# Kernel tuning notes

Hardware: AMD Instinct MI355X
Metric: run time of the kernel (lower is better)

## Reference

```python
import jax, jax.numpy as jnp
import numpy as np

VOCAB, HID, ADIM, B = 20, 128, 3, 32
NP, EP, NM, EM = 50000, 800000, 50000, 800000
IN_DIM = VOCAB + 3  # one-hot residues + 3D pos


def _gcn_conv(x, edge_index, W, b, n):
    # PyG GCNConv: h = XW; add self-loops; sym-normalized scatter-add; + bias
    h = x @ W
    loop = jnp.arange(n, dtype=edge_index.dtype)
    src = jnp.concatenate([edge_index[0], loop])
    dst = jnp.concatenate([edge_index[1], loop])
    deg = jax.ops.segment_sum(jnp.ones_like(dst, dtype=h.dtype), dst, num_segments=n)
    dinv = jnp.where(deg > 0, jax.lax.rsqrt(deg), 0.0)
    norm = dinv[src] * dinv[dst]  # [E+N]
    msg = h[src] * norm[:, None]  # [E+N, HID] dominant memory traffic
    return jax.ops.segment_sum(msg, dst, num_segments=n) + b


def _mean_pool(x, batch, nb):
    s = jax.ops.segment_sum(x, batch, num_segments=nb)
    c = jax.ops.segment_sum(jnp.ones((x.shape[0],), x.dtype), batch, num_segments=nb)
    return s / jnp.maximum(c, 1.0)[:, None]


def setup_inputs() -> dict:
    key = jax.random.key(0)
    ks = jax.random.split(key, 32)
    p = lambda k, shp: jax.random.normal(k, shp, dtype=jnp.float32) * 0.02
    inp = {
        "protein_residue": jax.random.randint(ks[0], (NP,), 0, VOCAB, dtype=jnp.int32),
        "protein_pos": jax.random.normal(ks[1], (NP, 3), dtype=jnp.float32),
        "protein_edge_index": jax.random.randint(ks[2], (2, EP), 0, NP, dtype=jnp.int32),
        "protein_batch": jnp.sort(jax.random.randint(ks[3], (NP,), 0, B, dtype=jnp.int32)),
        "molecule_residue": jax.random.randint(ks[4], (NM,), 0, VOCAB, dtype=jnp.int32),
        "molecule_pos": jax.random.normal(ks[5], (NM, 3), dtype=jnp.float32),
        "molecule_edge_index": jax.random.randint(ks[6], (2, EM), 0, NM, dtype=jnp.int32),
        "molecule_batch": jnp.sort(jax.random.randint(ks[7], (NM,), 0, B, dtype=jnp.int32)),
        "t": jax.random.randint(ks[8], (B,), 0, 1000, dtype=jnp.int32),
        "noisy_action": jax.random.normal(ks[9], (NM, ADIM), dtype=jnp.float32),
        # GCN params
        "Wp1": p(ks[10], (IN_DIM, HID)), "bp1": jnp.zeros((HID,), jnp.float32),
        "Wp2": p(ks[11], (HID, HID)),   "bp2": jnp.zeros((HID,), jnp.float32),
        "Wm1": p(ks[12], (IN_DIM, HID)), "bm1": jnp.zeros((HID,), jnp.float32),
        "Wm2": p(ks[13], (HID, HID)),   "bm2": jnp.zeros((HID,), jnp.float32),
        # timestep MLP
        "Wt1": p(ks[14], (1, HID)),   "bt1": jnp.zeros((HID,), jnp.float32),
        "Wt2": p(ks[15], (HID, HID)), "bt2": jnp.zeros((HID,), jnp.float32),
        # noise predictor: in = 2*HID + ADIM + HID = 387
        "Wn1": p(ks[16], (2 * HID + ADIM + HID, HID)), "bn1": jnp.zeros((HID,), jnp.float32),
        "Wn2": p(ks[17], (HID, ADIM)), "bn2": jnp.zeros((ADIM,), jnp.float32),
    }
    return inp


def reference(protein_residue, protein_pos, protein_edge_index, protein_batch,
              molecule_residue, molecule_pos, molecule_edge_index, molecule_batch,
              t, noisy_action,
              Wp1, bp1, Wp2, bp2, Wm1, bm1, Wm2, bm2,
              Wt1, bt1, Wt2, bt2, Wn1, bn1, Wn2, bn2):
    # protein branch
    x_p = jnp.concatenate([jax.nn.one_hot(protein_residue, VOCAB, dtype=jnp.float32), protein_pos], axis=1)
    x_p = jax.nn.relu(_gcn_conv(x_p, protein_edge_index, Wp1, bp1, NP))
    x_p = jax.nn.relu(_gcn_conv(x_p, protein_edge_index, Wp2, bp2, NP))
    protein_emb = _mean_pool(x_p, protein_batch, B)  # [B, HID]
    # molecule branch
    x_m = jnp.concatenate([jax.nn.one_hot(molecule_residue, VOCAB, dtype=jnp.float32), molecule_pos], axis=1)
    x_m = jax.nn.relu(_gcn_conv(x_m, molecule_edge_index, Wm1, bm1, NM))
    x_m = jax.nn.relu(_gcn_conv(x_m, molecule_edge_index, Wm2, bm2, NM))
    # timestep embedding
    t_emb = jax.nn.relu(t[:, None].astype(jnp.float32) @ Wt1 + bt1) @ Wt2 + bt2  # [B, HID]
    # gather pooled embeddings per molecule node, concat, MLP
    feat = jnp.concatenate([x_m, protein_emb[molecule_batch], t_emb[molecule_batch], noisy_action], axis=1)
    return jax.nn.relu(feat @ Wn1 + bn1) @ Wn2 + bn2  # [NM, ADIM]
```

## Files before the change

### kernel.cpp

```cpp
#include <hip/hip_runtime.h>
#include <hip/hip_bf16.h>

#define HID 128
#define BSH 7
#define CSRCAP 4096
#define PCHUNK 4096
#define HCHUNK 16384

typedef __attribute__((ext_vector_type(8))) short short8v;
typedef __attribute__((ext_vector_type(4))) float f32x4;
typedef __attribute__((ext_vector_type(2))) float f32x2;

#if defined(__has_builtin)
#if __has_builtin(__builtin_amdgcn_cvt_f32_fp8) && __has_builtin(__builtin_amdgcn_cvt_pk_fp8_f32)
#define HAVE_HW_FP8 1
#endif
#if __has_builtin(__builtin_amdgcn_cvt_pk_f32_fp8)
#define HAVE_HW_FP8_PK 1
#endif
#endif

__device__ __forceinline__ float4 f4fma(float a, float4 x, float4 y) {
    y.x += a * x.x; y.y += a * x.y; y.z += a * x.z; y.w += a * x.w; return y;
}
__device__ __forceinline__ unsigned f2bf2(float lo, float hi) {
    unsigned ul = __float_as_uint(lo), uh = __float_as_uint(hi);
    ul = (ul + 0x7FFF + ((ul >> 16) & 1)) >> 16;
    uh = (uh + 0x7FFF + ((uh >> 16) & 1)) & 0xFFFF0000u;
    return ul | uh;
}
__device__ __forceinline__ unsigned short f2bf1(float v) {
    unsigned u = __float_as_uint(v);
    u = (u + 0x7FFF + ((u >> 16) & 1)) >> 16;
    return (unsigned short)u;
}
__device__ __forceinline__ float bflo(unsigned u) { return __uint_as_float(u << 16); }
__device__ __forceinline__ float bfhi(unsigned u) { return __uint_as_float(u & 0xFFFF0000u); }
__device__ __forceinline__ float bf2f(unsigned short b) {
    return __uint_as_float(((unsigned)b) << 16);
}
__device__ __forceinline__ short8v zero8() {
    short8v z = {0, 0, 0, 0, 0, 0, 0, 0};
    return z;
}

#ifndef HAVE_HW_FP8
__device__ __forceinline__ unsigned fp8enc_pos(float a) {
    if (a >= 448.f) return 0x7Eu;
    if (a < 0.0009765625f) return 0u;
    unsigned b = __float_as_uint(a);
    int e = (int)(b >> 23) - 127;
    if (e >= -6) {
        unsigned r = b + 0x7FFFFu + ((b >> 20) & 1u);
        e = (int)(r >> 23) - 127;
        unsigned m = (r >> 20) & 7u;
        return ((unsigned)(e + 7) << 3) | m;
    } else {
        int m = (int)(a * 512.f + 0.5f);
        return (unsigned)m;
    }
}
__device__ __forceinline__ float fp8dec1(unsigned u7) {
    float fn = __uint_as_float((u7 + 0x3C0u) << 20);
    float fs = (float)u7 * 0.001953125f;
    return u7 >= 8 ? fn : fs;
}
#endif

__device__ __forceinline__ unsigned char enc1(float a) {
#ifdef HAVE_HW_FP8
    return (unsigned char)(__builtin_amdgcn_cvt_pk_fp8_f32(a, 0.f, 0, false) & 0xff);
#else
    return (unsigned char)fp8enc_pos(a);
#endif
}

__device__ __forceinline__ void dec16p(uint4 u, f32x2* v) {
#ifdef HAVE_HW_FP8_PK
    v[0] = __builtin_amdgcn_cvt_pk_f32_fp8((int)u.x, false);
    v[1] = __builtin_amdgcn_cvt_pk_f32_fp8((int)u.x, true);
    v[2] = __builtin_amdgcn_cvt_pk_f32_fp8((int)u.y, false);
    v[3] = __builtin_amdgcn_cvt_pk_f32_fp8((int)u.y, true);
    v[4] = __builtin_amdgcn_cvt_pk_f32_fp8((int)u.z, false);
    v[5] = __builtin_amdgcn_cvt_pk_f32_fp8((int)u.z, true);
    v[6] = __builtin_amdgcn_cvt_pk_f32_fp8((int)u.w, false);
    v[7] = __builtin_amdgcn_cvt_pk_f32_fp8((int)u.w, true);
#else
    unsigned w[4] = {u.x, u.y, u.z, u.w};
    #pragma unroll
    for (int k = 0; k < 4; ++k) {
        f32x2 a, b;
        a.x = fp8dec1(w[k] & 0xffu);         a.y = fp8dec1((w[k] >> 8) & 0xffu);
        b.x = fp8dec1((w[k] >> 16) & 0xffu); b.y = fp8dec1(w[k] >> 24);
        v[2 * k] = a; v[2 * k + 1] = b;
    }
#endif
}

__global__ __launch_bounds__(256) void k_bhist(const int* __restrict__ d1, int e1,
        const int* __restrict__ d2, int e2, int base2,
        int* __restrict__ bktcnt, long etot) {
    __shared__ int hist[1024];
    int tid = threadIdx.x;
    for (int b = tid; b < 1024; b += 256) hist[b] = 0;
    __syncthreads();
    long start = (long)blockIdx.x * HCHUNK;
    long end = start + HCHUNK; if (end > etot) end = etot;
    for (long i = start + tid; i < end; i += 256) {
        int d = (i < e1) ? d1[i] : d2[i - e1] + base2;
        atomicAdd(&hist[d >> BSH], 1);
    }
    __syncthreads();
    for (int b = tid; b < 1024; b += 256)
        if (hist[b]) atomicAdd(&bktcnt[b], hist[b]);
}

__global__ void k_bscan(const int* __restrict__ bktcnt, int* __restrict__ bofs,
                        int* __restrict__ bcur) {
    __shared__ int s[1024];
    int tid = threadIdx.x;
    int v = bktcnt[tid];
    s[tid] = v; __syncthreads();
    for (int o = 1; o < 1024; o <<= 1) {
        int t = (tid >= o) ? s[tid - o] : 0;
        __syncthreads();
        s[tid] += t;
        __syncthreads();
    }
    int ex = s[tid] - v;
    bofs[tid] = ex;
    bcur[tid] = ex;
    if (tid == 1023) bofs[1024] = s[1023];
}

__global__ __launch_bounds__(256) void k_part(
        const int* __restrict__ s1, const int* __restrict__ d1, int e1,
        const int* __restrict__ s2, const int* __restrict__ d2, int e2, int base2,
        int* __restrict__ bcur, int* __restrict__ pedge, int nb, long etot) {
    __shared__ int hist[1024];
    __shared__ int lofs[1024];
    __shared__ int gb[1024];
    __shared__ int ps[256];
    __shared__ int stage[PCHUNK];
    __shared__ unsigned short sbk[PCHUNK];
    int tid = threadIdx.x;
    long cbase = (long)blockIdx.x * PCHUNK;
    int cnt = (int)((etot - cbase) < PCHUNK ? (etot - cbase) : PCHUNK);
    for (int b = tid; b < 1024; b += 256) hist[b] = 0;
    __syncthreads();
    for (int i = tid; i < cnt; i += 256) {
        long e = cbase + i;
        int d = (e < e1) ? d1[e] : d2[e - e1] + base2;
        atomicAdd(&hist[d >> BSH], 1);
    }
    __syncthreads();
    int h0 = hist[tid * 4], h1 = hist[tid * 4 + 1], h2 = hist[tid * 4 + 2], h3 = hist[tid * 4 + 3];
    int sum = h0 + h1 + h2 + h3;
    ps[tid] = sum; __syncthreads();
    for (int o = 1; o < 256; o <<= 1) {
        int v = (tid >= o) ? ps[tid - o] : 0;
        __syncthreads();
        ps[tid] += v;
        __syncthreads();
    }
    int ex = ps[tid] - sum;
    lofs[tid * 4] = ex; lofs[tid * 4 + 1] = ex + h0;
    lofs[tid * 4 + 2] = ex + h0 + h1; lofs[tid * 4 + 3] = ex + h0 + h1 + h2;
    __syncthreads();
    for (int b = tid; b < nb; b += 256) {
        int c = hist[b];
        gb[b] = c ? atomicAdd(&bcur[b], c) : 0;
    }
    __syncthreads();
    for (int b = tid; b < 1024; b += 256) hist[b] = 0;
    __syncthreads();
    for (int i = tid; i < cnt; i += 256) {
        long e = cbase + i;
        int s, d;
        if (e < e1) { s = s1[e]; d = d1[e]; }
        else { s = s2[e - e1] + base2; d = d2[e - e1] + base2; }
        int b = d >> BSH;
        int p = lofs[b] + atomicAdd(&hist[b], 1);
        stage[p] = (s << BSH) | (d & ((1 << BSH) - 1));
        sbk[p] = (unsigned short)b;
    }
    __syncthreads();
    for (int i = tid; i < cnt; i += 256) {
        int b = sbk[i];
        pedge[gb[b] + (i - lofs[b])] = stage[i];
    }
}

__global__ __launch_bounds__(256) void k_csr(const int* __restrict__ pe,
        const int* __restrict__ bofs, int* __restrict__ csrs,
        int* __restrict__ deg, int* __restrict__ offs, float* __restrict__ dinv,
        const int* __restrict__ res1, const float* __restrict__ pos1,
        const int* __restrict__ res2, const float* __restrict__ pos2,
        int np, int np64, uint4* __restrict__ nrec, int n, int* __restrict__ bktcnt) {
    __shared__ int lofs2[128];
    __shared__ int lcnt[128];
    __shared__ int lcur[128];
    __shared__ int sc[128];
    __shared__ int ss[CSRCAP];
    int b = blockIdx.x, tid = threadIdx.x;
    int n0 = b << BSH;
    int nn = (n - n0) < 128 ? (n - n0) : 128;
    if (tid < 128) { lcnt[tid] = 0; lcur[tid] = 0; }
    __syncthreads();
    int base = bofs[b], total = bofs[b + 1] - base;
    for (int i = tid; i < total; i += 256)
        atomicAdd(&lcnt[pe[base + i] & ((1 << BSH) - 1)], 1);
    __syncthreads();
    int v = 0;
    if (tid < 128) { v = lcnt[tid]; sc[tid] = v; }
    __syncthreads();
    for (int o = 1; o < 128; o <<= 1) {
        int t = 0;
        if (tid < 128 && tid >= o) t = sc[tid - o];
        __syncthreads();
        if (tid < 128) sc[tid] += t;
        __syncthreads();
    }
    if (tid < 128) lofs2[tid] = sc[tid] - v;
    if (tid < nn) {
        int node = n0 + tid;
        offs[node] = base + sc[tid] - v;
        deg[node] = v;
        float dv = rsqrtf((float)(v + 1));
        dinv[node] = dv;
        const int* res = 0; const float* pos = 0; int bseg = 0; bool valid = false;
        if (node < np) { res = res1; pos = pos1; bseg = 0; valid = true; }
        else if (node >= np64) { res = res2; pos = pos2; bseg = np64; valid = true; }
        if (valid) {
            int lg = node - bseg;
            uint4 rr;
            rr.x = __float_as_uint(dv);
            rr.y = (unsigned)res[lg] | ((unsigned)f2bf1(pos[lg * 3 + 0]) << 16);
            rr.z = (unsigned)f2bf1(pos[lg * 3 + 1]) | ((unsigned)f2bf1(pos[lg * 3 + 2]) << 16);
            rr.w = 0;
            nrec[node] = rr;
        }
    }
    __syncthreads();
    if (total <= CSRCAP) {
        for (int i = tid; i < total; i += 256) {
            int e = pe[base + i];
            int ln = e & ((1 << BSH) - 1);
            int pos_ = lofs2[ln] + atomicAdd(&lcur[ln], 1);
            ss[pos_] = e >> BSH;
        }
        __syncthreads();
        for (int i = tid; i < total; i += 256) csrs[base + i] = ss[i];
    } else {
        for (int i = tid; i < total; i += 256) {
            int e = pe[base + i];
            int ln = e & ((1 << BSH) - 1);
            int pos_ = lofs2[ln] + atomicAdd(&lcur[ln], 1);
            csrs[base + pos_] = e >> BSH;
        }
    }
    if (b == 0)
        for (int i = tid; i < 1024; i += 256) bktcnt[i] = 0;
}

__global__ __launch_bounds__(256) void k_agg23c(
        const uint4* __restrict__ nrec, const int* __restrict__ offs,
        const int* __restrict__ deg, const int* __restrict__ csrs,
        int np, int np64, int nm, unsigned short* __restrict__ x23) {
    __shared__ float aggL[8][2][24];
    int grp = threadIdx.x >> 5, lane = threadIdx.x & 31;
    int g = blockIdx.x * 8 + grp;
    int ntot = np64 + nm;
    if (g >= ntot) return;
    bool valid = (g < np) || (g >= np64);
    if (!valid) {
        if (lane < 16) ((unsigned*)x23)[(size_t)g * 16 + lane] = 0;
        return;
    }
    int hf = lane >> 4;
    if (lane < 20) { aggL[grp][0][lane] = 0.f; aggL[grp][1][lane] = 0.f; }
    float sx = 0.f, sy = 0.f, sz = 0.f;
    int s0 = offs[g], m = deg[g];
    for (int i = lane; i < m; i += 32) {
        int s = csrs[s0 + i];
        uint4 r = nrec[s];
        float dv = __uint_as_float(r.x);
        int rs = (int)(r.y & 0xffffu);
        atomicAdd(&aggL[grp][hf][rs], dv);
        sx += dv * bfhi(r.y); sy += dv * bflo(r.z); sz += dv * bfhi(r.z);
    }
    uint4 sr = nrec[g];
    float dd = __uint_as_float(sr.x);
    if (lane == 0) atomicAdd(&aggL[grp][0][(int)(sr.y & 0xffffu)], dd);
    #pragma unroll
    for (int o = 1; o < 32; o <<= 1) {
        sx += __shfl_xor(sx, o, 32);
        sy += __shfl_xor(sy, o, 32);
        sz += __shfl_xor(sz, o, 32);
    }
    sx += dd * bfhi(sr.y); sy += dd * bflo(sr.z); sz += dd * bfhi(sr.z);
    float val = 0.f;
    if (lane < 20) val = aggL[grp][0][lane] + aggL[grp][1][lane];
    else if (lane == 20) val = sx;
    else if (lane == 21) val = sy;
    else if (lane == 22) val = sz;
    x23[(size_t)g * 32 + lane] = f2bf1(dd * val);
}

__global__ __launch_bounds__(256) void k_gemm1(const unsigned short* __restrict__ A,
        const unsigned short* __restrict__ Bt1, const unsigned short* __restrict__ Bt2,
        const float* __restrict__ b1a, const float* __restrict__ b1b,
        const float* __restrict__ dinv,
        int nb1, int np64, int ntot, unsigned* __restrict__ hb8) {
    __shared__ unsigned char stb[64][144];
    const int tid = threadIdx.x;
    const int wid = tid >> 6;
    const int lane = tid & 63;
    const int l15 = lane & 15, lg = lane >> 4;
    const unsigned short* Bt; const float* bb; int r0;
    if ((int)blockIdx.x < nb1) { Bt = Bt1; bb = b1a; r0 = blockIdx.x * 64; }
    else { Bt = Bt2; bb = b1b; r0 = np64 + ((int)blockIdx.x - nb1) * 64; }
    const int cbase = wid * 32;
    const int kb = lg * 8;
    f32x4 acc[4][2] = {};
    short8v b0 = *(const short8v*)&Bt[(size_t)(cbase + l15) * 32 + kb];
    short8v b1v = *(const short8v*)&Bt[(size_t)(cbase + 16 + l15) * 32 + kb];
    #pragma unroll
    for (int rt = 0; rt < 4; ++rt) {
        int gr = r0 + rt * 16 + l15;
        short8v a = (gr < ntot) ? *(const short8v*)&A[(size_t)gr * 32 + kb] : zero8();
        acc[rt][0] = __builtin_amdgcn_mfma_f32_16x16x32_bf16(a, b0, acc[rt][0], 0, 0, 0);
        acc[rt][1] = __builtin_amdgcn_mfma_f32_16x16x32_bf16(a, b1v, acc[rt][1], 0, 0, 0);
    }
    float bc0 = bb[cbase + l15], bc1 = bb[cbase + 16 + l15];
    #pragma unroll
    for (int rt = 0; rt < 4; ++rt)
        #pragma unroll
        for (int i = 0; i < 4; ++i) {
            int lr = rt * 16 + lg * 4 + i;
            int gr = r0 + lr;
            float dd16 = (gr < ntot) ? 16.f * dinv[gr] : 0.f;
            stb[lr][cbase + l15]      = enc1(dd16 * fmaxf(acc[rt][0][i] + bc0, 0.f));
            stb[lr][cbase + 16 + l15] = enc1(dd16 * fmaxf(acc[rt][1][i] + bc1, 0.f));
        }
    __syncthreads();
    #pragma unroll
    for (int h = 0; h < 2; ++h) {
        int idx = h * 256 + tid;
        int r = idx >> 3, q = idx & 7;
        int gr = r0 + r;
        if (gr < ntot)
            *(uint4*)&hb8[(size_t)gr * 32 + q * 4] = *(const uint4*)&stb[r][q * 16];
    }
}

__global__ __launch_bounds__(256) void k_agg(
        const uint4* __restrict__ H8, const int* __restrict__ offs,
        const int* __restrict__ deg, const int* __restrict__ csrs,
        const float* __restrict__ dinv,
        int np, int np64, int nm,
        unsigned short* __restrict__ outb) {
    int g = blockIdx.x * 8 + (threadIdx.x >> 5);
    if (g >= np && (g < np64 || g >= np64 + nm)) return;
    int lane = threadIdx.x & 31;
    int q = lane >> 3, l8 = lane & 7;
    f32x2 acc2[8];
    if (q == 0) {
        uint4 u = H8[(size_t)g * 8 + l8];
        dec16p(u, acc2);
    } else {
        #pragma unroll
        for (int c = 0; c < 8; ++c) { acc2[c].x = 0.f; acc2[c].y = 0.f; }
    }
    int s0 = offs[g], m = deg[g];
    for (int c0 = 0; c0 < m; c0 += 32) {
        int rem = m - c0; if (rem > 32) rem = 32;
        int li = lane < rem ? lane : rem - 1;
        int se = csrs[s0 + c0 + li];
        int nquad = (rem + 3) >> 2;
        #pragma unroll 8
        for (int j = 0; j < nquad; ++j) {
            int idx = j * 4 + q;
            bool act = idx < rem;
            int s = __shfl(se, act ? idx : 0, 32);
            uint4 u = H8[(size_t)s * 8 + l8];
            if (act) {
                f32x2 v[8]; dec16p(u, v);
                #pragma unroll
                for (int c = 0; c < 8; ++c) acc2[c] += v[c];
            }
        }
    }
    #pragma unroll
    for (int c = 0; c < 8; ++c) {
        acc2[c].x += __shfl_xor(acc2[c].x, 8, 32);
        acc2[c].y += __shfl_xor(acc2[c].y, 8, 32);
        acc2[c].x += __shfl_xor(acc2[c].x, 16, 32);
        acc2[c].y += __shfl_xor(acc2[c].y, 16, 32);
    }
    if (q == 0) {
        float di = dinv[g] * 0.0625f;
        uint4 pk0, pk1;
        pk0.x = f2bf2(di * acc2[0].x, di * acc2[0].y);
        pk0.y = f2bf2(di * acc2[1].x, di * acc2[1].y);
        pk0.z = f2bf2(di * acc2[2].x, di * acc2[2].y);
        pk0.w = f2bf2(di * acc2[3].x, di * acc2[3].y);
        pk1.x = f2bf2(di * acc2[4].x, di * acc2[4].y);
        pk1.y = f2bf2(di * acc2[5].x, di * acc2[5].y);
        pk1.z = f2bf2(di * acc2[6].x, di * acc2[6].y);
        pk1.w = f2bf2(di * acc2[7].x, di * acc2[7].y);
        *(uint4*)&outb[(size_t)g * HID + l8 * 16]     = pk0;
        *(uint4*)&outb[(size_t)g * HID + l8 * 16 + 8] = pk1;
    }
}

__global__ void k_tr(const float* __restrict__ Wa, const float* __restrict__ Wb,
                     const float* __restrict__ Wc,
                     unsigned short* __restrict__ Ta, unsigned short* __restrict__ Tb,
                     unsigned short* __restrict__ Tc,
                     const float* __restrict__ W1a, const float* __restrict__ W1b,
                     unsigned short* __restrict__ T1a, unsigned short* __restrict__ T1b,
                     int* __restrict__ bktcnt) {
    int b = blockIdx.x;
    int k = threadIdx.x;
    if (b == 0)
        for (int i = k; i < 1024; i += HID) bktcnt[i] = 0;
    if (b < 384) {
        int col = b & 127, m = b >> 7;
        const float* W = (m == 0) ? Wa : (m == 1 ? Wb : Wc);
        unsigned short* T = (m == 0) ? Ta : (m == 1 ? Tb : Tc);
        T[col * HID + k] = f2bf1(W[k * HID + col]);
    } else {
        int bb = b - 384;
        int col = bb & 127, seg = bb >> 7;
        const float* W = seg ? W1b : W1a;
        unsigned short* T = seg ? T1b : T1a;
        if (k < 32) T[col * 32 + k] = (k < 23) ? f2bf1(W[k * HID + col]) : (unsigned short)0;
    }
}

__global__ __launch_bounds__(256) void k_gemm(const unsigned short* __restrict__ A,
        const unsigned short* __restrict__ Bt1, const unsigned short* __restrict__ Bt2,
        const float* __restrict__ b2a, const float* __restrict__ b2b,
        int nb1, int np64, int ntot, unsigned short* __restrict__ C) {
    const int tid = threadIdx.x;
    const int wid = tid >> 6;
    const int lane = tid & 63;
    const int l15 = lane & 15, lg = lane >> 4;
    const unsigned short* Bt; const float* bb; int r0;
    if ((int)blockIdx.x < nb1) { Bt = Bt1; bb = b2a; r0 = blockIdx.x * 64; }
    else { Bt = Bt2; bb = b2b; r0 = np64 + ((int)blockIdx.x - nb1) * 64; }
    const int cbase = wid * 32;
    f32x4 acc[4][2] = {};
    #pragma unroll
    for (int ks = 0; ks < 4; ++ks) {
        int kb = ks * 32 + lg * 8;
        short8v b0 = *(const short8v*)&Bt[(size_t)(cbase + l15) * HID + kb];
        short8v b1 = *(const short8v*)&Bt[(size_t)(cbase + 16 + l15) * HID + kb];
        #pragma unroll
        for (int rt = 0; rt < 4; ++rt) {
            int gr = r0 + rt * 16 + l15;
            short8v a = (gr < ntot) ? *(const short8v*)&A[(size_t)gr * HID + kb] : zero8();
            acc[rt][0] = __builtin_amdgcn_mfma_f32_16x16x32_bf16(a, b0, acc[rt][0], 0, 0, 0);
            acc[rt][1] = __builtin_amdgcn_mfma_f32_16x16x32_bf16(a, b1, acc[rt][1], 0, 0, 0);
        }
    }
    float bc0 = bb[cbase + l15], bc1 = bb[cbase + 16 + l15];
    #pragma unroll
    for (int rt = 0; rt < 4; ++rt)
        #pragma unroll
        for (int i = 0; i < 4; ++i) {
            int gr = r0 + rt * 16 + lg * 4 + i;
            if (gr < ntot) {
                C[(size_t)gr * HID + cbase + l15]      = f2bf1(fmaxf(acc[rt][0][i] + bc0, 0.f));
                C[(size_t)gr * HID + cbase + 16 + l15] = f2bf1(fmaxf(acc[rt][1][i] + bc1, 0.f));
            }
        }
}

__global__ void k_pool(const unsigned short* __restrict__ x, const int* __restrict__ batch,
                       float* __restrict__ pool, int* __restrict__ cnt, int n) {
    const int ROWS = 64;
    int start = blockIdx.x * ROWS;
    if (start >= n) return;
    int end = start + ROWS; if (end > n) end = n;
    int c = threadIdx.x;
    float acc = 0.f;
    int cur = batch[start];
    int run = 0;
    for (int r = start; r < end; ++r) {
        int b = batch[r];
        if (b != cur) {
            atomicAdd(&pool[cur * HID + c], acc);
            if (c == 0) atomicAdd(&cnt[cur], run);
            acc = 0.f; run = 0; cur = b;
        }
        acc += bf2f(x[(size_t)r * HID + c]);
        run++;
    }
    atomicAdd(&pool[cur * HID + c], acc);
    if (c == 0) atomicAdd(&cnt[cur], run);
}

__global__ void k_combo2(const int* __restrict__ t, const float* __restrict__ Wt1,
                         const float* __restrict__ bt1, const float* __restrict__ Wt2,
                         const float* __restrict__ bt2,
                         const float* __restrict__ pool, const int* __restrict__ cntb,
                         const float* __restrict__ Wn1, const float* __restrict__ bn1,
                         float* __restrict__ combo) {
    __shared__ float th[HID];
    __shared__ float pe[HID];
    __shared__ float te[HID];
    int b = blockIdx.x, c = threadIdx.x;
    float tv = (float)t[b];
    float hv = tv * Wt1[c] + bt1[c];
    th[c] = hv > 0.f ? hv : 0.f;
    float dcnt = (float)cntb[b]; if (dcnt < 1.f) dcnt = 1.f;
    pe[c] = pool[b * HID + c] / dcnt;
    __syncthreads();
    float s = bt2[c];
    for (int k = 0; k < HID; ++k) s += th[k] * Wt2[k * HID + c];
    te[c] = s;
    __syncthreads();
    const float* Wp = Wn1 + 128 * HID;
    const float* Wt = Wn1 + 256 * HID;
    float o = bn1[c];
    for (int k = 0; k < HID; ++k)
        o += pe[k] * Wp[k * HID + c] + te[k] * Wt[k * HID + c];
    combo[b * HID + c] = o;
}

__global__ __launch_bounds__(256) void k_final(const unsigned short* __restrict__ A,
        const unsigned short* __restrict__ Bt ,
        const float* __restrict__ Wn1, const float* __restrict__ combo,
        const int* __restrict__ mbatch, const float* __restrict__ noisy,
        const float* __restrict__ Wn2, const float* __restrict__ bn2,
        float* __restrict__ out, int n) {
    __shared__ float hsm[64][132];
    const int tid = threadIdx.x;
    const int wid = tid >> 6;
    const int lane = tid & 63;
    const int l15 = lane & 15, lg = lane >> 4;
    const int r0 = blockIdx.x * 64;
    const int cbase = wid * 32;
    f32x4 acc[4][2] = {};
    #pragma unroll
    for (int ks = 0; ks < 4; ++ks) {
        int kb = ks * 32 + lg * 8;
        short8v b0 = *(const short8v*)&Bt[(size_t)(cbase + l15) * HID + kb];
        short8v b1 = *(const short8v*)&Bt[(size_t)(cbase + 16 + l15) * HID + kb];
        #pragma unroll
        for (int rt = 0; rt < 4; ++rt) {
            int gr = r0 + rt * 16 + l15;
            short8v a = (gr < n) ? *(const short8v*)&A[(size_t)gr * HID + kb] : zero8();
            acc[rt][0] = __builtin_amdgcn_mfma_f32_16x16x32_bf16(a, b0, acc[rt][0], 0, 0, 0);
            acc[rt][1] = __builtin_amdgcn_mfma_f32_16x16x32_bf16(a, b1, acc[rt][1], 0, 0, 0);
        }
    }
    const float* Wna = Wn1 + 384 * HID;
    #pragma unroll
    for (int rt = 0; rt < 4; ++rt)
        #pragma unroll
        for (int i = 0; i < 4; ++i) {
            int lr = rt * 16 + lg * 4 + i;
            int gr = r0 + lr;
            if (gr < n) {
                int b = mbatch[gr];
                float na0 = noisy[gr * 3 + 0], na1 = noisy[gr * 3 + 1], na2 = noisy[gr * 3 + 2];
                #pragma unroll
                for (int ct = 0; ct < 2; ++ct) {
                    int col = cbase + ct * 16 + l15;
                    float v = acc[rt][ct][i]
                            + na0 * Wna[col] + na1 * Wna[HID + col] + na2 * Wna[2 * HID + col]
                            + combo[b * HID + col];
                    hsm[lr][col] = v > 0.f ? v : 0.f;
                }
            }
        }
    __syncthreads();
    if (tid < 192) {
        int lr = tid / 3, j = tid - lr * 3;
        int gr = r0 + lr;
        if (gr < n) {
            float s = bn2[j];
            for (int c = 0; c < HID; ++c) s += hsm[lr][c] * Wn2[c * 3 + j];
            out[(size_t)gr * 3 + j] = s;
        }
    }
}

extern "C" void kernel_launch(void* const* d_in, const int* in_sizes, int n_in,
                              void* d_out, int out_size, void* d_ws, size_t ws_size,
                              hipStream_t stream) {
    const int*   p_res  = (const int*)d_in[0];
    const float* p_pos  = (const float*)d_in[1];
    const int*   p_ei   = (const int*)d_in[2];
    const int*   p_bat  = (const int*)d_in[3];
    const int*   m_res  = (const int*)d_in[4];
    const float* m_pos  = (const float*)d_in[5];
    const int*   m_ei   = (const int*)d_in[6];
    const int*   m_bat  = (const int*)d_in[7];
    const int*   t      = (const int*)d_in[8];
    const float* noisy  = (const float*)d_in[9];
    const float* Wp1 = (const float*)d_in[10], *bp1 = (const float*)d_in[11];
    const float* Wp2 = (const float*)d_in[12], *bp2 = (const float*)d_in[13];
    const float* Wm1 = (const float*)d_in[14], *bm1 = (const float*)d_in[15];
    const float* Wm2 = (const float*)d_in[16], *bm2 = (const float*)d_in[17];
    const float* Wt1 = (const float*)d_in[18], *bt1 = (const float*)d_in[19];
    const float* Wt2 = (const float*)d_in[20], *bt2 = (const float*)d_in[21];
    const float* Wn1 = (const float*)d_in[22], *bn1 = (const float*)d_in[23];
    const float* Wn2 = (const float*)d_in[24], *bn2 = (const float*)d_in[25];
    float* out = (float*)d_out;

    const int NP = in_sizes[0];
    const int EP = in_sizes[2] / 2;
    const int NM = in_sizes[4];
    const int EM = in_sizes[6] / 2;
    const int B  = in_sizes[8];
    auto al64 = [](int x) { return (x + 63) & ~63; };

    const int np64 = al64(NP);
    const long ntot_m = (long)np64 + NM;
    const long e2sum = (long)EP + EM;

    auto align256 = [](size_t x) { return (x + 255) & ~(size_t)255; };
    size_t req = 0;
    auto count = [&](size_t nb) { req = align256(req) + nb; };
    count(4ull * ntot_m);
    count(4ull * ntot_m);
    count(4ull * ntot_m);
    count(16ull * ntot_m);
    count(4ull * (1024 + 1025 + 1024));
    count(4ull * e2sum);
    count(4ull * e2sum);
    count(1ull * ntot_m * HID);
    count(2ull * ntot_m * HID);
    count(2ull * ntot_m * HID);
    count(2ull * (3 * HID * HID + 2 * HID * 32));
    count(4ull * (size_t)B * (HID + 1));
    count(4ull * (size_t)B * HID);
    bool merged = ws_size >= req + 4096;

    char* ws = (char*)d_ws;
    size_t off = 0;
    auto alloc = [&](size_t nb) { off = align256(off); size_t r = off; off += nb; return r; };

    const int NMAX = NP > NM ? NP : NM;
    const int EMAXs = EP > EM ? EP : EM;
    const long ntot_a = merged ? ntot_m : (long)al64(NMAX);
    const long etot_a = merged ? e2sum : (long)EMAXs;

    int*   deg  = (int*)(ws + alloc(4ull * ntot_a));
    int*   offs = (int*)(ws + alloc(4ull * ntot_a));
    float* dinv = (float*)(ws + alloc(4ull * ntot_a));
    uint4* nrec = (uint4*)(ws + alloc(16ull * ntot_a));
    int*   bktcnt = (int*)(ws + alloc(4ull * (1024 + 1025 + 1024)));
    int*   bofs = bktcnt + 1024;
    int*   bcur = bofs + 1025;
    int*   csre = (int*)(ws + alloc(4ull * etot_a));
    int*   csrs = (int*)(ws + alloc(4ull * etot_a));
    unsigned* hb8 = (unsigned*)(ws + alloc(1ull * ntot_a * HID));
    unsigned short* hb = (unsigned short*)(ws + alloc(2ull * ntot_a * HID));
    unsigned short* hc = (unsigned short*)(ws + alloc(2ull * ntot_a * HID));
    unsigned short* x23 = hc;
    unsigned short* w2ta = (unsigned short*)(ws + alloc(2ull * (3 * HID * HID + 2 * HID * 32)));
    unsigned short* w2tb = w2ta + HID * HID;
    unsigned short* wn1t = w2ta + 2 * HID * HID;
    unsigned short* w1ta = w2ta + 3 * HID * HID;
    unsigned short* w1tb = w1ta + HID * 32;
    float* pool = (float*)(ws + alloc(4ull * (size_t)B * (HID + 1)));
    int*   cntb = (int*)(pool + (size_t)B * HID);
    float* combo = (float*)(ws + alloc(4ull * (size_t)B * HID));

    k_tr<<<640, HID, 0, stream>>>(Wp2, Wm2, Wn1, w2ta, w2tb, wn1t, Wp1, Wm1, w1ta, w1tb,
                                  bktcnt);

    auto run = [&](int np_, int nm_,
                   const int* ei1, int e1, const int* ei2, int e2,
                   const int* res1, const float* pos1, const int* res2, const float* pos2,
                   const float* b1a, const float* b1b,
                   const unsigned short* w1A, const unsigned short* w1B,
                   const float* b2a, const float* b2b) {
        const int np64_ = al64(np_);
        const int ntot = np64_ + nm_;
        const long etot = (long)e1 + e2;
        const int nb = (ntot + 127) >> BSH;
        const int* s1 = ei1, *d1 = ei1 + e1;
        const int* s2 = ei2, *d2 = ei2 + e2;
        k_bhist<<<(int)((etot + HCHUNK - 1) / HCHUNK), 256, 0, stream>>>(
            d1, e1, d2, e2, np64_, bktcnt, etot);
        k_bscan<<<1, 1024, 0, stream>>>(bktcnt, bofs, bcur);
        k_part<<<(int)((etot + PCHUNK - 1) / PCHUNK), 256, 0, stream>>>(
            s1, d1, e1, s2, d2, e2, np64_, bcur, csre, nb, etot);
        k_csr<<<nb, 256, 0, stream>>>(csre, bofs, csrs, deg, offs, dinv,
                                      res1, pos1, res2, pos2, np_, np64_, nrec, ntot, bktcnt);
        k_agg23c<<<(ntot + 7) / 8, 256, 0, stream>>>(nrec, offs, deg, csrs,
                                                     np_, np64_, nm_, x23);
        const int nb1 = np64_ / 64;
        const int nb2 = (nm_ + 63) / 64;
        k_gemm1<<<nb1 + nb2, 256, 0, stream>>>(x23, w1A, w1B, b1a, b1b, dinv,
                                               nb1, np64_, ntot, hb8);
        k_agg<<<(ntot + 7) / 8, 256, 0, stream>>>((const uint4*)hb8, offs, deg, csrs, dinv,
                                                  np_, np64_, nm_, hc);
        k_gemm<<<nb1 + nb2, 256, 0, stream>>>(hc, w2ta, w2tb, b2a, b2b, nb1, np64_, ntot, hb);
    };

    if (merged) {
        run(NP, NM, p_ei, EP, m_ei, EM,
            p_res, p_pos, m_res, m_pos,
            bp1, bm1, w1ta, w1tb, bp2, bm2);
        hipMemsetAsync(pool, 0, 4ull * (size_t)B * (HID + 1), stream);
        k_pool<<<(NP + 63) / 64, HID, 0, stream>>>(hb, p_bat, pool, cntb, NP);
        k_combo2<<<B, HID, 0, stream>>>(t, Wt1, bt1, Wt2, bt2, pool, cntb, Wn1, bn1, combo);
        k_final<<<(NM + 63) / 64, 256, 0, stream>>>(hb + (size_t)np64 * HID, wn1t, Wn1, combo,
                                                    m_bat, noisy, Wn2, bn2, out, NM);
    } else {
        run(NP, 0, p_ei, EP, p_ei, 0,
            p_res, p_pos, p_res, p_pos,
            bp1, bp1, w1ta, w1ta, bp2, bp2);
        hipMemsetAsync(pool, 0, 4ull * (size_t)B * (HID + 1), stream);
        k_pool<<<(NP + 63) / 64, HID, 0, stream>>>(hb, p_bat, pool, cntb, NP);
        k_combo2<<<B, HID, 0, stream>>>(t, Wt1, bt1, Wt2, bt2, pool, cntb, Wn1, bn1, combo);
        run(0, NM, m_ei, 0, m_ei, EM,
            m_res, m_pos, m_res, m_pos,
            bm1, bm1, w1tb, w1tb, bm2, bm2);
        k_final<<<(NM + 63) / 64, 256, 0, stream>>>(hb, wn1t, Wn1, combo, m_bat, noisy,
                                                    Wn2, bn2, out, NM);
    }
}
```

Baseline: 225.3 us.

## Fold bucket scan into histogram kernel, drop pool memset, halve agg23c group width

The separate bucket prefix-scan kernel is removed: the last histogram block, found through an atomic done counter, performs the scan over 1024 buckets with 256 threads. The pool memset is folded into the weight-transpose kernel, and the counter is reset in k_csr. k_agg23c now uses 16-lane groups per node instead of 32, which halves the threads spent on low-degree nodes. Together these cut two launches or memsets per run and tighten the first aggregation, at the cost of a serial tail in the last histogram block and extra fence and atomic traffic.

```diff
diff --git a/kernel.cpp b/kernel.cpp
--- a/kernel.cpp
+++ b/kernel.cpp
@@ -99,8 +99,11 @@
 
 __global__ __launch_bounds__(256) void k_bhist(const int* __restrict__ d1, int e1,
         const int* __restrict__ d2, int e2, int base2,
-        int* __restrict__ bktcnt, long etot) {
+        int* __restrict__ bktcnt, int* __restrict__ bofs, int* __restrict__ bcur,
+        int* __restrict__ done, int nblocks, long etot) {
     __shared__ int hist[1024];
+    __shared__ int ps[256];
+    __shared__ int lastflag;
     int tid = threadIdx.x;
     for (int b = tid; b < 1024; b += 256) hist[b] = 0;
     __syncthreads();
@@ -113,24 +116,27 @@
     __syncthreads();
     for (int b = tid; b < 1024; b += 256)
         if (hist[b]) atomicAdd(&bktcnt[b], hist[b]);
-}
-
-__global__ void k_bscan(const int* __restrict__ bktcnt, int* __restrict__ bofs,
-                        int* __restrict__ bcur) {
-    __shared__ int s[1024];
-    int tid = threadIdx.x;
-    int v = bktcnt[tid];
-    s[tid] = v; __syncthreads();
-    for (int o = 1; o < 1024; o <<= 1) {
-        int t = (tid >= o) ? s[tid - o] : 0;
+    __threadfence();
+    if (tid == 0) lastflag = (atomicAdd(done, 1) == nblocks - 1);
+    __syncthreads();
+    if (!lastflag) return;
+    __threadfence();
+    int b4 = tid * 4;
+    int h0 = bktcnt[b4], h1 = bktcnt[b4 + 1], h2 = bktcnt[b4 + 2], h3 = bktcnt[b4 + 3];
+    int sum = h0 + h1 + h2 + h3;
+    ps[tid] = sum; __syncthreads();
+    for (int o = 1; o < 256; o <<= 1) {
+        int v = (tid >= o) ? ps[tid - o] : 0;
         __syncthreads();
-        s[tid] += t;
+        ps[tid] += v;
         __syncthreads();
     }
-    int ex = s[tid] - v;
-    bofs[tid] = ex;
-    bcur[tid] = ex;
-    if (tid == 1023) bofs[1024] = s[1023];
+    int ex = ps[tid] - sum;
+    bofs[b4] = ex; bcur[b4] = ex;
+    bofs[b4 + 1] = ex + h0; bcur[b4 + 1] = ex + h0;
+    bofs[b4 + 2] = ex + h0 + h1; bcur[b4 + 2] = ex + h0 + h1;
+    bofs[b4 + 3] = ex + h0 + h1 + h2; bcur[b4 + 3] = ex + h0 + h1 + h2;
+    if (tid == 255) bofs[1024] = ps[255];
 }
 
 __global__ __launch_bounds__(256) void k_part(
@@ -196,7 +202,8 @@
         int* __restrict__ deg, int* __restrict__ offs, float* __restrict__ dinv,
         const int* __restrict__ res1, const float* __restrict__ pos1,
         const int* __restrict__ res2, const float* __restrict__ pos2,
-        int np, int np64, uint4* __restrict__ nrec, int n, int* __restrict__ bktcnt) {
+        int np, int np64, uint4* __restrict__ nrec, int n,
+        int* __restrict__ bktcnt, int* __restrict__ done) {
     __shared__ int lofs2[128];
     __shared__ int lcnt[128];
     __shared__ int lcur[128];
@@ -259,52 +266,59 @@
             csrs[base + pos_] = e >> BSH;
         }
     }
-    if (b == 0)
+    if (b == 0) {
         for (int i = tid; i < 1024; i += 256) bktcnt[i] = 0;
+        if (tid == 0) *done = 0;
+    }
 }
 
 __global__ __launch_bounds__(256) void k_agg23c(
         const uint4* __restrict__ nrec, const int* __restrict__ offs,
         const int* __restrict__ deg, const int* __restrict__ csrs,
         int np, int np64, int nm, unsigned short* __restrict__ x23) {
-    __shared__ float aggL[8][2][24];
-    int grp = threadIdx.x >> 5, lane = threadIdx.x & 31;
-    int g = blockIdx.x * 8 + grp;
+    __shared__ float aggL[16][24];
+    int grp = threadIdx.x >> 4, lane = threadIdx.x & 15;
+    int g = blockIdx.x * 16 + grp;
     int ntot = np64 + nm;
     if (g >= ntot) return;
     bool valid = (g < np) || (g >= np64);
     if (!valid) {
-        if (lane < 16) ((unsigned*)x23)[(size_t)g * 16 + lane] = 0;
+        ((unsigned*)x23)[(size_t)g * 16 + lane] = 0;
         return;
     }
-    int hf = lane >> 4;
-    if (lane < 20) { aggL[grp][0][lane] = 0.f; aggL[grp][1][lane] = 0.f; }
+    if (lane < 12) { aggL[grp][lane] = 0.f; aggL[grp][lane + 12] = 0.f; }
     float sx = 0.f, sy = 0.f, sz = 0.f;
     int s0 = offs[g], m = deg[g];
-    for (int i = lane; i < m; i += 32) {
+    for (int i = lane; i < m; i += 16) {
         int s = csrs[s0 + i];
         uint4 r = nrec[s];
         float dv = __uint_as_float(r.x);
         int rs = (int)(r.y & 0xffffu);
-        atomicAdd(&aggL[grp][hf][rs], dv);
+        atomicAdd(&aggL[grp][rs], dv);
         sx += dv * bfhi(r.y); sy += dv * bflo(r.z); sz += dv * bfhi(r.z);
     }
     uint4 sr = nrec[g];
     float dd = __uint_as_float(sr.x);
-    if (lane == 0) atomicAdd(&aggL[grp][0][(int)(sr.y & 0xffffu)], dd);
-    #pragma unroll
-    for (int o = 1; o < 32; o <<= 1) {
-        sx += __shfl_xor(sx, o, 32);
-        sy += __shfl_xor(sy, o, 32);
-        sz += __shfl_xor(sz, o, 32);
+    if (lane == 0) atomicAdd(&aggL[grp][(int)(sr.y & 0xffffu)], dd);
+    #pragma unroll
+    for (int o = 1; o < 16; o <<= 1) {
+        sx += __shfl_xor(sx, o, 16);
+        sy += __shfl_xor(sy, o, 16);
+        sz += __shfl_xor(sz, o, 16);
     }
     sx += dd * bfhi(sr.y); sy += dd * bflo(sr.z); sz += dd * bfhi(sr.z);
-    float val = 0.f;
-    if (lane < 20) val = aggL[grp][0][lane] + aggL[grp][1][lane];
-    else if (lane == 20) val = sx;
-    else if (lane == 21) val = sy;
-    else if (lane == 22) val = sz;
-    x23[(size_t)g * 32 + lane] = f2bf1(dd * val);
+    float v0 = (lane < 20) ? aggL[grp][lane] : 0.f;
+    int i1 = lane + 16;
+    float v1;
+    if (i1 < 20) v1 = aggL[grp][i1];
+    else if (i1 == 20) v1 = sx;
+    else if (i1 == 21) v1 = sy;
+    else if (i1 == 22) v1 = sz;
+    else v1 = 0.f;
+    unsigned pk = ((unsigned)f2bf1(dd * v0)) | (((unsigned)f2bf1(dd * v1)) << 16);
+    x23[(size_t)g * 32 + lane]      = f2bf1(dd * v0);
+    x23[(size_t)g * 32 + lane + 16] = f2bf1(dd * v1);
+    (void)pk;
 }
 
 __global__ __launch_bounds__(256) void k_gemm1(const unsigned short* __restrict__ A,
@@ -420,11 +434,16 @@
                      unsigned short* __restrict__ Tc,
                      const float* __restrict__ W1a, const float* __restrict__ W1b,
                      unsigned short* __restrict__ T1a, unsigned short* __restrict__ T1b,
-                     int* __restrict__ bktcnt) {
+                     int* __restrict__ bktcnt, int* __restrict__ done,
+                     float* __restrict__ pool, int pooln) {
     int b = blockIdx.x;
     int k = threadIdx.x;
-    if (b == 0)
+    if (b == 0) {
         for (int i = k; i < 1024; i += HID) bktcnt[i] = 0;
+        if (k == 0) *done = 0;
+    } else if (b == 1) {
+        for (int i = k; i < pooln; i += HID) pool[i] = 0.f;
+    }
     if (b < 384) {
         int col = b & 127, m = b >> 7;
         const float* W = (m == 0) ? Wa : (m == 1 ? Wb : Wc);
@@ -630,7 +649,7 @@
     count(4ull * ntot_m);
     count(4ull * ntot_m);
     count(16ull * ntot_m);
-    count(4ull * (1024 + 1025 + 1024));
+    count(4ull * (1024 + 1025 + 1024 + 1));
     count(4ull * e2sum);
     count(4ull * e2sum);
     count(1ull * ntot_m * HID);
@@ -654,9 +673,10 @@
     int*   offs = (int*)(ws + alloc(4ull * ntot_a));
     float* dinv = (float*)(ws + alloc(4ull * ntot_a));
     uint4* nrec = (uint4*)(ws + alloc(16ull * ntot_a));
-    int*   bktcnt = (int*)(ws + alloc(4ull * (1024 + 1025 + 1024)));
+    int*   bktcnt = (int*)(ws + alloc(4ull * (1024 + 1025 + 1024 + 1)));
     int*   bofs = bktcnt + 1024;
     int*   bcur = bofs + 1025;
+    int*   done = bcur + 1024;
     int*   csre = (int*)(ws + alloc(4ull * etot_a));
     int*   csrs = (int*)(ws + alloc(4ull * etot_a));
     unsigned* hb8 = (unsigned*)(ws + alloc(1ull * ntot_a * HID));
@@ -673,7 +693,7 @@
     float* combo = (float*)(ws + alloc(4ull * (size_t)B * HID));
 
     k_tr<<<640, HID, 0, stream>>>(Wp2, Wm2, Wn1, w2ta, w2tb, wn1t, Wp1, Wm1, w1ta, w1tb,
-                                  bktcnt);
+                                  bktcnt, done, pool, B * (HID + 1));
 
     auto run = [&](int np_, int nm_,
                    const int* ei1, int e1, const int* ei2, int e2,
@@ -687,15 +707,16 @@
         const int nb = (ntot + 127) >> BSH;
         const int* s1 = ei1, *d1 = ei1 + e1;
         const int* s2 = ei2, *d2 = ei2 + e2;
-        k_bhist<<<(int)((etot + HCHUNK - 1) / HCHUNK), 256, 0, stream>>>(
-            d1, e1, d2, e2, np64_, bktcnt, etot);
-        k_bscan<<<1, 1024, 0, stream>>>(bktcnt, bofs, bcur);
+        const int nhb = (int)((etot + HCHUNK - 1) / HCHUNK);
+        k_bhist<<<nhb, 256, 0, stream>>>(d1, e1, d2, e2, np64_, bktcnt, bofs, bcur,
+                                         done, nhb, etot);
         k_part<<<(int)((etot + PCHUNK - 1) / PCHUNK), 256, 0, stream>>>(
             s1, d1, e1, s2, d2, e2, np64_, bcur, csre, nb, etot);
         k_csr<<<nb, 256, 0, stream>>>(csre, bofs, csrs, deg, offs, dinv,
-                                      res1, pos1, res2, pos2, np_, np64_, nrec, ntot, bktcnt);
-        k_agg23c<<<(ntot + 7) / 8, 256, 0, stream>>>(nrec, offs, deg, csrs,
-                                                     np_, np64_, nm_, x23);
+                                      res1, pos1, res2, pos2, np_, np64_, nrec, ntot,
+                                      bktcnt, done);
+        k_agg23c<<<(ntot + 15) / 16, 256, 0, stream>>>(nrec, offs, deg, csrs,
+                                                       np_, np64_, nm_, x23);
         const int nb1 = np64_ / 64;
         const int nb2 = (nm_ + 63) / 64;
         k_gemm1<<<nb1 + nb2, 256, 0, stream>>>(x23, w1A, w1B, b1a, b1b, dinv,
@@ -709,7 +730,6 @@
         run(NP, NM, p_ei, EP, m_ei, EM,
             p_res, p_pos, m_res, m_pos,
             bp1, bm1, w1ta, w1tb, bp2, bm2);
-        hipMemsetAsync(pool, 0, 4ull * (size_t)B * (HID + 1), stream);
         k_pool<<<(NP + 63) / 64, HID, 0, stream>>>(hb, p_bat, pool, cntb, NP);
         k_combo2<<<B, HID, 0, stream>>>(t, Wt1, bt1, Wt2, bt2, pool, cntb, Wn1, bn1, combo);
         k_final<<<(NM + 63) / 64, 256, 0, stream>>>(hb + (size_t)np64 * HID, wn1t, Wn1, combo,
@@ -718,7 +738,6 @@
         run(NP, 0, p_ei, EP, p_ei, 0,
             p_res, p_pos, p_res, p_pos,
             bp1, bp1, w1ta, w1ta, bp2, bp2);
-        hipMemsetAsync(pool, 0, 4ull * (size_t)B * (HID + 1), stream);
         k_pool<<<(NP + 63) / 64, HID, 0, stream>>>(hb, p_bat, pool, cntb, NP);
         k_combo2<<<B, HID, 0, stream>>>(t, Wt1, bt1, Wt2, bt2, pool, cntb, Wn1, bn1, combo);
         run(0, NM, m_ei, 0, m_ei, EM,
```

After: 222.0 us. No clear change (-1.5%).
